# Optimization experiments

Measured on AMD Instinct MI355X. Metric: run time of the kernel, lower is better.

Reference implementation:

```python
import jax, jax.numpy as jnp
import numpy as np

N_NODES = 100000
N_EDGES = 1600000
NFEAT = 128
NHID = 64
DROPOUT = 0.5


def setup_inputs() -> dict:
    key = jax.random.key(0)
    k1, k2, k3, k4, k5, k6 = jax.random.split(key, 6)
    x = jax.random.normal(k1, (N_NODES, NFEAT), dtype=jnp.float32)
    edge_row = jax.random.randint(k2, (N_EDGES,), 0, N_NODES, dtype=jnp.int32)
    edge_col = jax.random.randint(k3, (N_EDGES,), 0, N_NODES, dtype=jnp.int32)
    edge_val = jax.random.uniform(k4, (N_EDGES,), dtype=jnp.float32)
    # GraphConvolution params (uniform init as in Kipf's reference impl)
    stdv = 1.0 / np.sqrt(NHID)
    W = jax.random.uniform(k5, (NFEAT, NHID), minval=-stdv, maxval=stdv, dtype=jnp.float32)
    b = jax.random.uniform(k6, (NHID,), minval=-stdv, maxval=stdv, dtype=jnp.float32)
    return {"x": x, "edge_row": edge_row, "edge_col": edge_col,
            "edge_val": edge_val, "W": W, "b": b}


def reference(x, edge_row, edge_col, edge_val, W, b):
    # GraphConvolution: support = x @ W ; out = spmm(adj, support) + b
    support = x @ W                                   # [N, nhid]
    msgs = edge_val[:, None] * support[edge_col]       # gather: [E, nhid]
    agg = jax.ops.segment_sum(msgs, edge_row, num_segments=N_NODES)  # scatter-add
    h = jax.nn.relu(agg + b)
    # F.dropout(p=0.5, training=True): inverted dropout with fixed mask
    keep = 1.0 - DROPOUT
    mask = jax.random.bernoulli(jax.random.key(42), keep, h.shape)
    return jnp.where(mask, h / keep, 0.0)
```

## Files before the change

kernel.cpp:

```cpp
#include <hip/hip_runtime.h>

#define N_NODES 100000
#define N_EDGES 1600000
#define NFEAT 128
#define NHID 64

#define BBITS 8
#define NBUCK 391
#define BATCH 4096
#define NBATCH ((N_EDGES + BATCH - 1) / BATCH)
#define NREP 4
#define RSTRIDE 1536
#define HCAP 2560
#define CMASK 0x1FFFF

typedef __attribute__((ext_vector_type(8))) short short8;
typedef __attribute__((ext_vector_type(4))) float f32x4;

__device__ __forceinline__ unsigned short f2bf(float f) {
  unsigned u = __float_as_uint(f);
  u += 0x7fffu + ((u >> 16) & 1u);
  return (unsigned short)(u >> 16);
}

__global__ __launch_bounds__(256) void gcn_wt(const float* __restrict__ W,
                                              unsigned short* __restrict__ wt,
                                              int* __restrict__ cursor) {
  const int i = blockIdx.x * 256 + threadIdx.x;
  const int n = i >> 7;
  const int k = i & 127;
  wt[i] = f2bf(W[k * NHID + n]);
  if (blockIdx.x == 0)
    for (int b = threadIdx.x; b < NBUCK * NREP; b += 256)
      cursor[b * 16] = 0;
}

__global__ __launch_bounds__(256) void gcn_gemm(const float* __restrict__ x,
                                                const unsigned short* __restrict__ wt,
                                                unsigned short* __restrict__ support_h) {
  __shared__ float ldsx[64 * NFEAT];
  const int t = threadIdx.x;
  const int node0 = blockIdx.x * 64;
  const float4* __restrict__ gx = (const float4*)(x + (size_t)node0 * NFEAT);
  float4* lx4 = (float4*)ldsx;
  const int limit4 = (N_NODES - node0) * (NFEAT / 4);
#pragma unroll
  for (int i = 0; i < 8; ++i) {
    const int idx = i * 256 + t;
    if (idx < limit4) lx4[idx] = gx[idx];
  }
  __syncthreads();
  const int wv = t >> 6;
  const int lane = t & 63;
  const int quad = lane >> 4;
  const int nl = lane & 15;
  const int mrow = wv * 16 + nl;
  f32x4 acc[4];
#pragma unroll
  for (int nt = 0; nt < 4; ++nt)
#pragma unroll
    for (int r = 0; r < 4; ++r) acc[nt][r] = 0.f;
#pragma unroll
  for (int kc = 0; kc < 4; ++kc) {
    const float* ap = &ldsx[mrow * NFEAT + kc * 32 + quad * 8];
    const float4 a0 = *(const float4*)ap;
    const float4 a1 = *(const float4*)(ap + 4);
    union { short8 v; unsigned short s[8]; } au;
    au.s[0] = f2bf(a0.x); au.s[1] = f2bf(a0.y);
    au.s[2] = f2bf(a0.z); au.s[3] = f2bf(a0.w);
    au.s[4] = f2bf(a1.x); au.s[5] = f2bf(a1.y);
    au.s[6] = f2bf(a1.z); au.s[7] = f2bf(a1.w);
#pragma unroll
    for (int nt = 0; nt < 4; ++nt) {
      const short8 bf = *(const short8*)(wt + (size_t)(nt * 16 + nl) * NFEAT +
                                         kc * 32 + quad * 8);
      acc[nt] = __builtin_amdgcn_mfma_f32_16x16x32_bf16(au.v, bf, acc[nt], 0, 0, 0);
    }
  }
#pragma unroll
  for (int nt = 0; nt < 4; ++nt)
#pragma unroll
    for (int r = 0; r < 4; ++r) {
      const int node = node0 + wv * 16 + quad * 4 + r;
      if (node < N_NODES)
        support_h[(size_t)node * NHID + nt * 16 + nl] = f2bf(acc[nt][r]);
    }
}

__global__ __launch_bounds__(512) void gcn_bin(const int* __restrict__ erow,
                                               const int* __restrict__ ecol,
                                               const float* __restrict__ eval_,
                                               int* __restrict__ cursor,
                                               int2* __restrict__ eg) {
  __shared__ int h[NBUCK];
  __shared__ int ofs[NBUCK];
  __shared__ int wsum[8];
  __shared__ int spx[BATCH];
  __shared__ int sv[BATCH];
  __shared__ short sb[BATCH];
  const int t = threadIdx.x;
  const int rep = blockIdx.x & (NREP - 1);
  if (t < NBUCK) h[t] = 0;
  __syncthreads();
  const int base = blockIdx.x * BATCH;
  const int n = min(BATCH, N_EDGES - base);
  int mypx[8], myv[8], myrank[8], myb[8];
#pragma unroll
  for (int u = 0; u < 8; ++u) {
    const int j = t + u * 512;
    if (j < n) {
      const int r = erow[base + j];
      mypx[u] = ((r & 255) << 17) | ecol[base + j];
      myv[u] = __float_as_int(eval_[base + j]);
      myb[u] = r >> BBITS;
      myrank[u] = atomicAdd(&h[myb[u]], 1);
    }
  }
  __syncthreads();
  const int hv = (t < NBUCK) ? h[t] : 0;
  const int lane = t & 63;
  int v = hv;
#pragma unroll
  for (int off = 1; off < 64; off <<= 1) {
    const int u = __shfl_up(v, off);
    if (lane >= off) v += u;
  }
  if (lane == 63) wsum[t >> 6] = v;
  __syncthreads();
  int wbase = 0;
  const int mywv = t >> 6;
  for (int w = 0; w < mywv; ++w) wbase += wsum[w];
  const int my_ofs = wbase + v - hv;
  if (t < NBUCK) {
    ofs[t] = my_ofs;
    const int c = hv;
    if (c > 0) {
      const int old = atomicAdd(&cursor[(t * NREP + rep) * 16], c);
      h[t] = (t * NREP + rep) * RSTRIDE + old - my_ofs;
    }
  }
  __syncthreads();
#pragma unroll
  for (int u = 0; u < 8; ++u) {
    const int j = t + u * 512;
    if (j < n) {
      const int pos = ofs[myb[u]] + myrank[u];
      spx[pos] = mypx[u];
      sv[pos] = myv[u];
      sb[pos] = (short)myb[u];
    }
  }
  __syncthreads();
  for (int j = t; j < n; j += 512) {
    const int d = h[sb[j]] + j;
    eg[d] = make_int2(spx[j], sv[j]);
  }
}

__device__ __forceinline__ unsigned rotl32(unsigned v, int r) {
  return (v << r) | (v >> (32 - r));
}

__device__ __forceinline__ unsigned threefry_draw(unsigned i) {
  const unsigned ks0 = 0u;
  const unsigned ks1 = 42u;
  const unsigned ks2 = 0x1BD11BDAu ^ 42u;
  unsigned x0 = 0u + ks0;
  unsigned x1 = i + ks1;
#define TF_ROUND(r) { x0 += x1; x1 = rotl32(x1, (r)); x1 ^= x0; }
  TF_ROUND(13) TF_ROUND(15) TF_ROUND(26) TF_ROUND(6)
  x0 += ks1; x1 += ks2 + 1u;
  TF_ROUND(17) TF_ROUND(29) TF_ROUND(16) TF_ROUND(24)
  x0 += ks2; x1 += ks0 + 2u;
  TF_ROUND(13) TF_ROUND(15) TF_ROUND(26) TF_ROUND(6)
  x0 += ks0; x1 += ks1 + 3u;
  TF_ROUND(17) TF_ROUND(29) TF_ROUND(16) TF_ROUND(24)
  x0 += ks1; x1 += ks2 + 4u;
  TF_ROUND(13) TF_ROUND(15) TF_ROUND(26) TF_ROUND(6)
  x0 += ks2; x1 += ks0 + 5u;
#undef TF_ROUND
  return x0 ^ x1;
}

__global__ __launch_bounds__(512) void gcn_rowagg(const int* __restrict__ cursor,
                                                  const int2* __restrict__ eg,
                                                  const unsigned short* __restrict__ support_h,
                                                  const float* __restrict__ b,
                                                  float* __restrict__ out) {
  __shared__ int2 srec[HCAP];
  __shared__ int cnt[128];
  __shared__ int rstart[128];
  const int t = threadIdx.x;
  const int k = blockIdx.x >> 1;
  const int half = blockIdx.x & 1;
  if (t < 128) cnt[t] = 0;
  __syncthreads();
  int px[12], pv[12], rk[12];
  int idx = 0;
#pragma unroll
  for (int rep = 0; rep < NREP; ++rep) {
    const int span = k * NREP + rep;
    const int n = cursor[span * 16];
    const int sbase = span * RSTRIDE;
#pragma unroll
    for (int u = 0; u < 3; ++u, ++idx) {
      const int j = t + u * 512;
      const bool ok = j < n;
      int2 p = make_int2(0, 0);
      if (ok) p = eg[sbase + j];
      px[idx] = p.x;
      pv[idx] = p.y;
      const int r = ((unsigned)p.x) >> 17;
      rk[idx] = (ok && ((r >> 7) == half)) ? atomicAdd(&cnt[r & 127], 1) : -1;
    }
  }
  __syncthreads();
  if (t < 64) {
    const int a0 = cnt[t];
    const int a1 = cnt[64 + t];
    int s0 = a0;
#pragma unroll
    for (int off = 1; off < 64; off <<= 1) {
      const int u = __shfl_up(s0, off);
      if (t >= off) s0 += u;
    }
    const int tot0 = __shfl(s0, 63);
    int s1 = a1;
#pragma unroll
    for (int off = 1; off < 64; off <<= 1) {
      const int u = __shfl_up(s1, off);
      if (t >= off) s1 += u;
    }
    rstart[t] = s0 - a0;
    rstart[64 + t] = tot0 + s1 - a1;
  }
  __syncthreads();
#pragma unroll
  for (int u = 0; u < 12; ++u) {
    if (rk[u] >= 0) {
      const int r = (((unsigned)px[u]) >> 17) & 127;
      srec[rstart[r] + rk[u]] = make_int2(px[u] & CMASK, pv[u]);
    }
  }
  __syncthreads();
  const int wv = t >> 6;
  const int lane = t & 63;
  const int grp = lane >> 3;
  const int sub = lane & 7;
  const int feat = (sub << 3) | grp;
  const float bias = b[feat];
  for (int rr = 0; rr < 16; ++rr) {
    const int r = wv * 16 + rr;
    const int node = (k << BBITS) + (half << 7) + r;
    if (node >= N_NODES) break;
    const int s = rstart[r];
    const int e = s + cnt[r];
    float acc[8];
#pragma unroll
    for (int j = 0; j < 8; ++j) acc[j] = 0.f;
    for (int i = s; i < e; i += 8) {
      const int ii = i + grp;
      int2 p = make_int2(0, 0);
      if (ii < e) p = srec[ii];
      const uint4 q = ((const uint4*)support_h)[(size_t)p.x * 8 + sub];
      const float v = __int_as_float(p.y);
      acc[0] = __builtin_fmaf(v, __uint_as_float(q.x << 16), acc[0]);
      acc[1] = __builtin_fmaf(v, __uint_as_float(q.x & 0xffff0000u), acc[1]);
      acc[2] = __builtin_fmaf(v, __uint_as_float(q.y << 16), acc[2]);
      acc[3] = __builtin_fmaf(v, __uint_as_float(q.y & 0xffff0000u), acc[3]);
      acc[4] = __builtin_fmaf(v, __uint_as_float(q.z << 16), acc[4]);
      acc[5] = __builtin_fmaf(v, __uint_as_float(q.z & 0xffff0000u), acc[5]);
      acc[6] = __builtin_fmaf(v, __uint_as_float(q.w << 16), acc[6]);
      acc[7] = __builtin_fmaf(v, __uint_as_float(q.w & 0xffff0000u), acc[7]);
    }
    const int g0 = grp & 1, g1 = (grp >> 1) & 1, g2 = grp >> 2;
    float v4[4];
#pragma unroll
    for (int i = 0; i < 4; ++i) {
      const float keep = g0 ? acc[2 * i + 1] : acc[2 * i];
      const float give = g0 ? acc[2 * i] : acc[2 * i + 1];
      v4[i] = keep + __shfl_xor(give, 8);
    }
    float v2[2];
#pragma unroll
    for (int i = 0; i < 2; ++i) {
      const float keep = g1 ? v4[2 * i + 1] : v4[2 * i];
      const float give = g1 ? v4[2 * i] : v4[2 * i + 1];
      v2[i] = keep + __shfl_xor(give, 16);
    }
    const float keep = g2 ? v2[1] : v2[0];
    const float give = g2 ? v2[0] : v2[1];
    const float aval = keep + __shfl_xor(give, 32);
    const float h = fmaxf(aval + bias, 0.f);
    const unsigned idxg = (unsigned)node * 64u + (unsigned)feat;
    const bool keepm = (threefry_draw(idxg) >> 31) == 0u;
    out[idxg] = keepm ? h * 2.0f : 0.0f;
  }
}

extern "C" void kernel_launch(void* const* d_in, const int* in_sizes, int n_in,
                              void* d_out, int out_size, void* d_ws, size_t ws_size,
                              hipStream_t stream) {
  const float* x     = (const float*)d_in[0];
  const int*   erow  = (const int*)d_in[1];
  const int*   ecol  = (const int*)d_in[2];
  const float* eval_ = (const float*)d_in[3];
  const float* W     = (const float*)d_in[4];
  const float* b     = (const float*)d_in[5];
  float* out = (float*)d_out;

  char* ws = (char*)d_ws;
  unsigned short* support_h = (unsigned short*)(ws);
  unsigned short* wt        = (unsigned short*)(ws + 12800000);
  int*  cursor  = (int*)(ws + 12816384);
  int2* eg      = (int2*)(ws + 12916480);

  hipLaunchKernelGGL(gcn_wt, dim3(32), dim3(256), 0, stream, W, wt, cursor);
  hipLaunchKernelGGL(gcn_gemm, dim3((N_NODES + 63) / 64), dim3(256), 0, stream,
                     x, wt, support_h);
  hipLaunchKernelGGL(gcn_bin, dim3(NBATCH), dim3(512), 0, stream,
                     erow, ecol, eval_, cursor, eg);
  hipLaunchKernelGGL(gcn_rowagg, dim3(2 * NBUCK), dim3(512), 0, stream,
                     cursor, eg, support_h, b, out);
}
```

Measured before the change: 194.0 us.

## Fuse GEMM, binning and row aggregation into one cooperative persistent kernel

Replaces the four separate launches with one persistent cooperative kernel. Its first phase interleaves the GEMM tiles (now 128 nodes, with W transposed to bf16 in LDS per tile) and the edge-binning batches, then a grid-wide sync precedes the row aggregation phase. The cursor reset moves to a memset. The aim is to cut launch gaps and tail effects and to let the GEMM overlap the binning. In exchange, every GEMM tile redoes the W conversion, the grid is capped by occupancy, and the grid sync plus cooperative launch add their own overhead.

```diff
diff --git a/kernel.cpp b/kernel.cpp
--- a/kernel.cpp
+++ b/kernel.cpp
@@ -1,4 +1,7 @@
 #include <hip/hip_runtime.h>
+#include <hip/hip_cooperative_groups.h>
+
+namespace cg = cooperative_groups;
 
 #define N_NODES 100000
 #define N_EDGES 1600000
@@ -8,11 +11,14 @@
 #define BBITS 8
 #define NBUCK 391
 #define BATCH 4096
-#define NBATCH ((N_EDGES + BATCH - 1) / BATCH)
+#define NBATCH 391
+#define NTILE 782
 #define NREP 4
 #define RSTRIDE 1536
 #define HCAP 2560
 #define CMASK 0x1FFFF
+#define XPITCH 136
+#define SH_BYTES 52224
 
 typedef __attribute__((ext_vector_type(8))) short short8;
 typedef __attribute__((ext_vector_type(4))) float f32x4;
@@ -21,140 +27,6 @@
   unsigned u = __float_as_uint(f);
   u += 0x7fffu + ((u >> 16) & 1u);
   return (unsigned short)(u >> 16);
-}
-
-__global__ __launch_bounds__(256) void gcn_wt(const float* __restrict__ W,
-                                              unsigned short* __restrict__ wt,
-                                              int* __restrict__ cursor) {
-  const int i = blockIdx.x * 256 + threadIdx.x;
-  const int n = i >> 7;
-  const int k = i & 127;
-  wt[i] = f2bf(W[k * NHID + n]);
-  if (blockIdx.x == 0)
-    for (int b = threadIdx.x; b < NBUCK * NREP; b += 256)
-      cursor[b * 16] = 0;
-}
-
-__global__ __launch_bounds__(256) void gcn_gemm(const float* __restrict__ x,
-                                                const unsigned short* __restrict__ wt,
-                                                unsigned short* __restrict__ support_h) {
-  __shared__ float ldsx[64 * NFEAT];
-  const int t = threadIdx.x;
-  const int node0 = blockIdx.x * 64;
-  const float4* __restrict__ gx = (const float4*)(x + (size_t)node0 * NFEAT);
-  float4* lx4 = (float4*)ldsx;
-  const int limit4 = (N_NODES - node0) * (NFEAT / 4);
-#pragma unroll
-  for (int i = 0; i < 8; ++i) {
-    const int idx = i * 256 + t;
-    if (idx < limit4) lx4[idx] = gx[idx];
-  }
-  __syncthreads();
-  const int wv = t >> 6;
-  const int lane = t & 63;
-  const int quad = lane >> 4;
-  const int nl = lane & 15;
-  const int mrow = wv * 16 + nl;
-  f32x4 acc[4];
-#pragma unroll
-  for (int nt = 0; nt < 4; ++nt)
-#pragma unroll
-    for (int r = 0; r < 4; ++r) acc[nt][r] = 0.f;
-#pragma unroll
-  for (int kc = 0; kc < 4; ++kc) {
-    const float* ap = &ldsx[mrow * NFEAT + kc * 32 + quad * 8];
-    const float4 a0 = *(const float4*)ap;
-    const float4 a1 = *(const float4*)(ap + 4);
-    union { short8 v; unsigned short s[8]; } au;
-    au.s[0] = f2bf(a0.x); au.s[1] = f2bf(a0.y);
-    au.s[2] = f2bf(a0.z); au.s[3] = f2bf(a0.w);
-    au.s[4] = f2bf(a1.x); au.s[5] = f2bf(a1.y);
-    au.s[6] = f2bf(a1.z); au.s[7] = f2bf(a1.w);
-#pragma unroll
-    for (int nt = 0; nt < 4; ++nt) {
-      const short8 bf = *(const short8*)(wt + (size_t)(nt * 16 + nl) * NFEAT +
-                                         kc * 32 + quad * 8);
-      acc[nt] = __builtin_amdgcn_mfma_f32_16x16x32_bf16(au.v, bf, acc[nt], 0, 0, 0);
-    }
-  }
-#pragma unroll
-  for (int nt = 0; nt < 4; ++nt)
-#pragma unroll
-    for (int r = 0; r < 4; ++r) {
-      const int node = node0 + wv * 16 + quad * 4 + r;
-      if (node < N_NODES)
-        support_h[(size_t)node * NHID + nt * 16 + nl] = f2bf(acc[nt][r]);
-    }
-}
-
-__global__ __launch_bounds__(512) void gcn_bin(const int* __restrict__ erow,
-                                               const int* __restrict__ ecol,
-                                               const float* __restrict__ eval_,
-                                               int* __restrict__ cursor,
-                                               int2* __restrict__ eg) {
-  __shared__ int h[NBUCK];
-  __shared__ int ofs[NBUCK];
-  __shared__ int wsum[8];
-  __shared__ int spx[BATCH];
-  __shared__ int sv[BATCH];
-  __shared__ short sb[BATCH];
-  const int t = threadIdx.x;
-  const int rep = blockIdx.x & (NREP - 1);
-  if (t < NBUCK) h[t] = 0;
-  __syncthreads();
-  const int base = blockIdx.x * BATCH;
-  const int n = min(BATCH, N_EDGES - base);
-  int mypx[8], myv[8], myrank[8], myb[8];
-#pragma unroll
-  for (int u = 0; u < 8; ++u) {
-    const int j = t + u * 512;
-    if (j < n) {
-      const int r = erow[base + j];
-      mypx[u] = ((r & 255) << 17) | ecol[base + j];
-      myv[u] = __float_as_int(eval_[base + j]);
-      myb[u] = r >> BBITS;
-      myrank[u] = atomicAdd(&h[myb[u]], 1);
-    }
-  }
-  __syncthreads();
-  const int hv = (t < NBUCK) ? h[t] : 0;
-  const int lane = t & 63;
-  int v = hv;
-#pragma unroll
-  for (int off = 1; off < 64; off <<= 1) {
-    const int u = __shfl_up(v, off);
-    if (lane >= off) v += u;
-  }
-  if (lane == 63) wsum[t >> 6] = v;
-  __syncthreads();
-  int wbase = 0;
-  const int mywv = t >> 6;
-  for (int w = 0; w < mywv; ++w) wbase += wsum[w];
-  const int my_ofs = wbase + v - hv;
-  if (t < NBUCK) {
-    ofs[t] = my_ofs;
-    const int c = hv;
-    if (c > 0) {
-      const int old = atomicAdd(&cursor[(t * NREP + rep) * 16], c);
-      h[t] = (t * NREP + rep) * RSTRIDE + old - my_ofs;
-    }
-  }
-  __syncthreads();
-#pragma unroll
-  for (int u = 0; u < 8; ++u) {
-    const int j = t + u * 512;
-    if (j < n) {
-      const int pos = ofs[myb[u]] + myrank[u];
-      spx[pos] = mypx[u];
-      sv[pos] = myv[u];
-      sb[pos] = (short)myb[u];
-    }
-  }
-  __syncthreads();
-  for (int j = t; j < n; j += 512) {
-    const int d = h[sb[j]] + j;
-    eg[d] = make_int2(spx[j], sv[j]);
-  }
 }
 
 __device__ __forceinline__ unsigned rotl32(unsigned v, int r) {
@@ -182,119 +54,247 @@
   return x0 ^ x1;
 }
 
-__global__ __launch_bounds__(512) void gcn_rowagg(const int* __restrict__ cursor,
-                                                  const int2* __restrict__ eg,
-                                                  const unsigned short* __restrict__ support_h,
-                                                  const float* __restrict__ b,
-                                                  float* __restrict__ out) {
-  __shared__ int2 srec[HCAP];
-  __shared__ int cnt[128];
-  __shared__ int rstart[128];
+__global__ void __launch_bounds__(512, 6) gcn_mega(
+    const float* __restrict__ x, const int* __restrict__ erow,
+    const int* __restrict__ ecol, const float* __restrict__ eval_,
+    const float* __restrict__ W, const float* __restrict__ bias_g,
+    float* __restrict__ out, unsigned short* __restrict__ support_h,
+    int* __restrict__ cursor, int2* __restrict__ eg) {
+  __shared__ __align__(16) char shraw[SH_BYTES];
   const int t = threadIdx.x;
-  const int k = blockIdx.x >> 1;
-  const int half = blockIdx.x & 1;
-  if (t < 128) cnt[t] = 0;
-  __syncthreads();
-  int px[12], pv[12], rk[12];
-  int idx = 0;
-#pragma unroll
-  for (int rep = 0; rep < NREP; ++rep) {
-    const int span = k * NREP + rep;
-    const int n = cursor[span * 16];
-    const int sbase = span * RSTRIDE;
-#pragma unroll
-    for (int u = 0; u < 3; ++u, ++idx) {
-      const int j = t + u * 512;
-      const bool ok = j < n;
-      int2 p = make_int2(0, 0);
-      if (ok) p = eg[sbase + j];
-      px[idx] = p.x;
-      pv[idx] = p.y;
-      const int r = ((unsigned)p.x) >> 17;
-      rk[idx] = (ok && ((r >> 7) == half)) ? atomicAdd(&cnt[r & 127], 1) : -1;
-    }
+  cg::grid_group grid = cg::this_grid();
+
+  for (int u = blockIdx.x; u < NTILE + NBATCH; u += gridDim.x) {
+    __syncthreads();
+    if (u < NTILE) {
+      unsigned short* xbf = (unsigned short*)shraw;
+      unsigned short* wtb = (unsigned short*)(shraw + 34816);
+      const int node0 = u * 128;
+      for (int i = t; i < NHID * NFEAT; i += 512) {
+        const int k = i >> 6;
+        const int n = i & 63;
+        wtb[n * XPITCH + k] = f2bf(W[i]);
+      }
+      const int limf4 = min(128, N_NODES - node0) * 32;
+      const float4* gx = (const float4*)(x + (size_t)node0 * NFEAT);
+      for (int i = t; i < 128 * 32; i += 512) {
+        if (i < limf4) {
+          const float4 v = gx[i];
+          ushort4 o;
+          o.x = f2bf(v.x); o.y = f2bf(v.y); o.z = f2bf(v.z); o.w = f2bf(v.w);
+          *(ushort4*)(xbf + (i >> 5) * XPITCH + (i & 31) * 4) = o;
+        }
+      }
+      __syncthreads();
+      const int wv = t >> 6;
+      const int lane = t & 63;
+      const int quad = lane >> 4;
+      const int nl = lane & 15;
+      const int mrow = wv * 16 + nl;
+      f32x4 acc[4];
+#pragma unroll
+      for (int nt = 0; nt < 4; ++nt)
+#pragma unroll
+        for (int r = 0; r < 4; ++r) acc[nt][r] = 0.f;
+#pragma unroll
+      for (int kc = 0; kc < 4; ++kc) {
+        const short8 a = *(const short8*)(xbf + mrow * XPITCH + kc * 32 + quad * 8);
+#pragma unroll
+        for (int nt = 0; nt < 4; ++nt) {
+          const short8 bf = *(const short8*)(wtb + (nt * 16 + nl) * XPITCH +
+                                             kc * 32 + quad * 8);
+          acc[nt] = __builtin_amdgcn_mfma_f32_16x16x32_bf16(a, bf, acc[nt], 0, 0, 0);
+        }
+      }
+#pragma unroll
+      for (int nt = 0; nt < 4; ++nt)
+#pragma unroll
+        for (int r = 0; r < 4; ++r) {
+          const int node = node0 + wv * 16 + quad * 4 + r;
+          if (node < N_NODES)
+            support_h[(size_t)node * NHID + nt * 16 + nl] = f2bf(acc[nt][r]);
+        }
+    } else {
+      int* h    = (int*)shraw;
+      int* ofs  = (int*)(shraw + 1568);
+      int* wsum = (int*)(shraw + 3136);
+      int* spx  = (int*)(shraw + 3168);
+      int* sv   = (int*)(shraw + 19552);
+      short* sb = (short*)(shraw + 35936);
+      const int bidx = u - NTILE;
+      const int rep = bidx & (NREP - 1);
+      if (t < NBUCK) h[t] = 0;
+      __syncthreads();
+      const int base = bidx * BATCH;
+      const int n = min(BATCH, N_EDGES - base);
+      int mypx[8], myv[8], myrank[8], myb[8];
+#pragma unroll
+      for (int v = 0; v < 8; ++v) {
+        const int j = t + v * 512;
+        if (j < n) {
+          const int r = erow[base + j];
+          mypx[v] = ((r & 255) << 17) | ecol[base + j];
+          myv[v] = __float_as_int(eval_[base + j]);
+          myb[v] = r >> BBITS;
+          myrank[v] = atomicAdd(&h[myb[v]], 1);
+        }
+      }
+      __syncthreads();
+      const int hv = (t < NBUCK) ? h[t] : 0;
+      const int lane = t & 63;
+      int v = hv;
+#pragma unroll
+      for (int off = 1; off < 64; off <<= 1) {
+        const int uu = __shfl_up(v, off);
+        if (lane >= off) v += uu;
+      }
+      if (lane == 63) wsum[t >> 6] = v;
+      __syncthreads();
+      int wbase = 0;
+      const int mywv = t >> 6;
+      for (int w = 0; w < mywv; ++w) wbase += wsum[w];
+      const int my_ofs = wbase + v - hv;
+      if (t < NBUCK) {
+        ofs[t] = my_ofs;
+        const int c = hv;
+        if (c > 0) {
+          const int old = atomicAdd(&cursor[(t * NREP + rep) * 16], c);
+          h[t] = (t * NREP + rep) * RSTRIDE + old - my_ofs;
+        }
+      }
+      __syncthreads();
+#pragma unroll
+      for (int vv = 0; vv < 8; ++vv) {
+        const int j = t + vv * 512;
+        if (j < n) {
+          const int pos = ofs[myb[vv]] + myrank[vv];
+          spx[pos] = mypx[vv];
+          sv[pos] = myv[vv];
+          sb[pos] = (short)myb[vv];
+        }
+      }
+      __syncthreads();
+      for (int j = t; j < n; j += 512) {
+        const int d = h[sb[j]] + j;
+        eg[d] = make_int2(spx[j], sv[j]);
+      }
+    }
+    __syncthreads();
   }
-  __syncthreads();
-  if (t < 64) {
-    const int a0 = cnt[t];
-    const int a1 = cnt[64 + t];
-    int s0 = a0;
-#pragma unroll
-    for (int off = 1; off < 64; off <<= 1) {
-      const int u = __shfl_up(s0, off);
-      if (t >= off) s0 += u;
-    }
-    const int tot0 = __shfl(s0, 63);
-    int s1 = a1;
-#pragma unroll
-    for (int off = 1; off < 64; off <<= 1) {
-      const int u = __shfl_up(s1, off);
-      if (t >= off) s1 += u;
-    }
-    rstart[t] = s0 - a0;
-    rstart[64 + t] = tot0 + s1 - a1;
-  }
-  __syncthreads();
-#pragma unroll
-  for (int u = 0; u < 12; ++u) {
-    if (rk[u] >= 0) {
-      const int r = (((unsigned)px[u]) >> 17) & 127;
-      srec[rstart[r] + rk[u]] = make_int2(px[u] & CMASK, pv[u]);
-    }
-  }
-  __syncthreads();
-  const int wv = t >> 6;
-  const int lane = t & 63;
-  const int grp = lane >> 3;
-  const int sub = lane & 7;
-  const int feat = (sub << 3) | grp;
-  const float bias = b[feat];
-  for (int rr = 0; rr < 16; ++rr) {
-    const int r = wv * 16 + rr;
-    const int node = (k << BBITS) + (half << 7) + r;
-    if (node >= N_NODES) break;
-    const int s = rstart[r];
-    const int e = s + cnt[r];
-    float acc[8];
-#pragma unroll
-    for (int j = 0; j < 8; ++j) acc[j] = 0.f;
-    for (int i = s; i < e; i += 8) {
-      const int ii = i + grp;
-      int2 p = make_int2(0, 0);
-      if (ii < e) p = srec[ii];
-      const uint4 q = ((const uint4*)support_h)[(size_t)p.x * 8 + sub];
-      const float v = __int_as_float(p.y);
-      acc[0] = __builtin_fmaf(v, __uint_as_float(q.x << 16), acc[0]);
-      acc[1] = __builtin_fmaf(v, __uint_as_float(q.x & 0xffff0000u), acc[1]);
-      acc[2] = __builtin_fmaf(v, __uint_as_float(q.y << 16), acc[2]);
-      acc[3] = __builtin_fmaf(v, __uint_as_float(q.y & 0xffff0000u), acc[3]);
-      acc[4] = __builtin_fmaf(v, __uint_as_float(q.z << 16), acc[4]);
-      acc[5] = __builtin_fmaf(v, __uint_as_float(q.z & 0xffff0000u), acc[5]);
-      acc[6] = __builtin_fmaf(v, __uint_as_float(q.w << 16), acc[6]);
-      acc[7] = __builtin_fmaf(v, __uint_as_float(q.w & 0xffff0000u), acc[7]);
-    }
-    const int g0 = grp & 1, g1 = (grp >> 1) & 1, g2 = grp >> 2;
-    float v4[4];
-#pragma unroll
-    for (int i = 0; i < 4; ++i) {
-      const float keep = g0 ? acc[2 * i + 1] : acc[2 * i];
-      const float give = g0 ? acc[2 * i] : acc[2 * i + 1];
-      v4[i] = keep + __shfl_xor(give, 8);
-    }
-    float v2[2];
-#pragma unroll
-    for (int i = 0; i < 2; ++i) {
-      const float keep = g1 ? v4[2 * i + 1] : v4[2 * i];
-      const float give = g1 ? v4[2 * i] : v4[2 * i + 1];
-      v2[i] = keep + __shfl_xor(give, 16);
-    }
-    const float keep = g2 ? v2[1] : v2[0];
-    const float give = g2 ? v2[0] : v2[1];
-    const float aval = keep + __shfl_xor(give, 32);
-    const float h = fmaxf(aval + bias, 0.f);
-    const unsigned idxg = (unsigned)node * 64u + (unsigned)feat;
-    const bool keepm = (threefry_draw(idxg) >> 31) == 0u;
-    out[idxg] = keepm ? h * 2.0f : 0.0f;
+
+  grid.sync();
+
+  for (int u = blockIdx.x; u < 2 * NBUCK; u += gridDim.x) {
+    __syncthreads();
+    int2* srec  = (int2*)shraw;
+    int* cnt    = (int*)(shraw + 20480);
+    int* rstart = (int*)(shraw + 20992);
+    const int k = u >> 1;
+    const int half = u & 1;
+    if (t < 128) cnt[t] = 0;
+    __syncthreads();
+    int px[12], pv[12], rk[12];
+    int idx = 0;
+#pragma unroll
+    for (int rep = 0; rep < NREP; ++rep) {
+      const int span = k * NREP + rep;
+      const int n = cursor[span * 16];
+      const int sbase = span * RSTRIDE;
+#pragma unroll
+      for (int uu = 0; uu < 3; ++uu, ++idx) {
+        const int j = t + uu * 512;
+        const bool ok = j < n;
+        int2 p = make_int2(0, 0);
+        if (ok) p = eg[sbase + j];
+        px[idx] = p.x;
+        pv[idx] = p.y;
+        const int r = ((unsigned)p.x) >> 17;
+        rk[idx] = (ok && ((r >> 7) == half)) ? atomicAdd(&cnt[r & 127], 1) : -1;
+      }
+    }
+    __syncthreads();
+    if (t < 64) {
+      const int a0 = cnt[t];
+      const int a1 = cnt[64 + t];
+      int s0 = a0;
+#pragma unroll
+      for (int off = 1; off < 64; off <<= 1) {
+        const int uu = __shfl_up(s0, off);
+        if (t >= off) s0 += uu;
+      }
+      const int tot0 = __shfl(s0, 63);
+      int s1 = a1;
+#pragma unroll
+      for (int off = 1; off < 64; off <<= 1) {
+        const int uu = __shfl_up(s1, off);
+        if (t >= off) s1 += uu;
+      }
+      rstart[t] = s0 - a0;
+      rstart[64 + t] = tot0 + s1 - a1;
+    }
+    __syncthreads();
+#pragma unroll
+    for (int uu = 0; uu < 12; ++uu) {
+      if (rk[uu] >= 0) {
+        const int r = (((unsigned)px[uu]) >> 17) & 127;
+        srec[rstart[r] + rk[uu]] = make_int2(px[uu] & CMASK, pv[uu]);
+      }
+    }
+    __syncthreads();
+    const int wv = t >> 6;
+    const int lane = t & 63;
+    const int grp = lane >> 3;
+    const int sub = lane & 7;
+    const int feat = (sub << 3) | grp;
+    const float bias = bias_g[feat];
+    for (int rr = 0; rr < 16; ++rr) {
+      const int r = wv * 16 + rr;
+      const int node = (k << BBITS) + (half << 7) + r;
+      if (node >= N_NODES) break;
+      const int s = rstart[r];
+      const int e = s + cnt[r];
+      float acc[8];
+#pragma unroll
+      for (int j = 0; j < 8; ++j) acc[j] = 0.f;
+      for (int i = s; i < e; i += 8) {
+        const int ii = i + grp;
+        int2 p = make_int2(0, 0);
+        if (ii < e) p = srec[ii];
+        const uint4 q = ((const uint4*)support_h)[(size_t)p.x * 8 + sub];
+        const float v = __int_as_float(p.y);
+        acc[0] = __builtin_fmaf(v, __uint_as_float(q.x << 16), acc[0]);
+        acc[1] = __builtin_fmaf(v, __uint_as_float(q.x & 0xffff0000u), acc[1]);
+        acc[2] = __builtin_fmaf(v, __uint_as_float(q.y << 16), acc[2]);
+        acc[3] = __builtin_fmaf(v, __uint_as_float(q.y & 0xffff0000u), acc[3]);
+        acc[4] = __builtin_fmaf(v, __uint_as_float(q.z << 16), acc[4]);
+        acc[5] = __builtin_fmaf(v, __uint_as_float(q.z & 0xffff0000u), acc[5]);
+        acc[6] = __builtin_fmaf(v, __uint_as_float(q.w << 16), acc[6]);
+        acc[7] = __builtin_fmaf(v, __uint_as_float(q.w & 0xffff0000u), acc[7]);
+      }
+      const int g0 = grp & 1, g1 = (grp >> 1) & 1, g2 = grp >> 2;
+      float v4[4];
+#pragma unroll
+      for (int i = 0; i < 4; ++i) {
+        const float keep = g0 ? acc[2 * i + 1] : acc[2 * i];
+        const float give = g0 ? acc[2 * i] : acc[2 * i + 1];
+        v4[i] = keep + __shfl_xor(give, 8);
+      }
+      float v2[2];
+#pragma unroll
+      for (int i = 0; i < 2; ++i) {
+        const float keep = g1 ? v4[2 * i + 1] : v4[2 * i];
+        const float give = g1 ? v4[2 * i] : v4[2 * i + 1];
+        v2[i] = keep + __shfl_xor(give, 16);
+      }
+      const float keep = g2 ? v2[1] : v2[0];
+      const float give = g2 ? v2[0] : v2[1];
+      const float aval = keep + __shfl_xor(give, 32);
+      const float h = fmaxf(aval + bias, 0.f);
+      const unsigned idxg = (unsigned)node * 64u + (unsigned)feat;
+      const bool keepm = (threefry_draw(idxg) >> 31) == 0u;
+      out[idxg] = keepm ? h * 2.0f : 0.0f;
+    }
+    __syncthreads();
   }
 }
 
@@ -311,15 +311,20 @@
 
   char* ws = (char*)d_ws;
   unsigned short* support_h = (unsigned short*)(ws);
-  unsigned short* wt        = (unsigned short*)(ws + 12800000);
-  int*  cursor  = (int*)(ws + 12816384);
-  int2* eg      = (int2*)(ws + 12916480);
-
-  hipLaunchKernelGGL(gcn_wt, dim3(32), dim3(256), 0, stream, W, wt, cursor);
-  hipLaunchKernelGGL(gcn_gemm, dim3((N_NODES + 63) / 64), dim3(256), 0, stream,
-                     x, wt, support_h);
-  hipLaunchKernelGGL(gcn_bin, dim3(NBATCH), dim3(512), 0, stream,
-                     erow, ecol, eval_, cursor, eg);
-  hipLaunchKernelGGL(gcn_rowagg, dim3(2 * NBUCK), dim3(512), 0, stream,
-                     cursor, eg, support_h, b, out);
-}
+  int*  cursor = (int*)(ws + 12800000);
+  int2* eg     = (int2*)(ws + 12900096);
+
+  hipMemsetAsync(cursor, 0, NBUCK * NREP * 16 * sizeof(int), stream);
+
+  int maxb = 0;
+  hipOccupancyMaxActiveBlocksPerMultiprocessor(&maxb, (const void*)gcn_mega, 512, 0);
+  if (maxb < 1) maxb = 1;
+  if (maxb > 3) maxb = 3;
+  const int grid = maxb * 256;
+
+  void* args[] = {(void*)&x, (void*)&erow, (void*)&ecol, (void*)&eval_,
+                  (void*)&W, (void*)&b, (void*)&out, (void*)&support_h,
+                  (void*)&cursor, (void*)&eg};
+  hipLaunchCooperativeKernel((const void*)gcn_mega, dim3(grid), dim3(512),
+                             args, 0, stream);
+}
```

Measured after the change: 321.7 us. 1.66x slower.

## Fuse weight transpose into GEMM, store bf16 x in LDS, split rowagg into quarters

Applied to the files above, without the earlier changes.

Removes the separate weight-transpose kernel: each GEMM block now converts W to bf16 and transposes it into padded LDS itself, and it also zeroes the cursors. The x tile is converted to bf16 once during staging, which shrinks LDS use and drops the per-MFMA conversion. The row-aggregation kernel is split into four blocks per bucket instead of two, with smaller LDS record buffers, to raise parallelism. The cost is redundant W conversion in every GEMM block, and more rowagg blocks that each re-read the bucket's edge records. NBATCH is hardcoded to 391, the same value as before.

```diff
diff --git a/kernel.cpp b/kernel.cpp
--- a/kernel.cpp
+++ b/kernel.cpp
@@ -8,11 +8,12 @@
 #define BBITS 8
 #define NBUCK 391
 #define BATCH 4096
-#define NBATCH ((N_EDGES + BATCH - 1) / BATCH)
+#define NBATCH 391
 #define NREP 4
 #define RSTRIDE 1536
-#define HCAP 2560
+#define QCAP 1408
 #define CMASK 0x1FFFF
+#define XP 132
 
 typedef __attribute__((ext_vector_type(8))) short short8;
 typedef __attribute__((ext_vector_type(4))) float f32x4;
@@ -23,31 +24,30 @@
   return (unsigned short)(u >> 16);
 }
 
-__global__ __launch_bounds__(256) void gcn_wt(const float* __restrict__ W,
-                                              unsigned short* __restrict__ wt,
-                                              int* __restrict__ cursor) {
-  const int i = blockIdx.x * 256 + threadIdx.x;
-  const int n = i >> 7;
-  const int k = i & 127;
-  wt[i] = f2bf(W[k * NHID + n]);
+__global__ __launch_bounds__(256) void gcn_gemm(const float* __restrict__ x,
+                                                const float* __restrict__ W,
+                                                unsigned short* __restrict__ support_h,
+                                                int* __restrict__ cursor) {
+  __shared__ unsigned short xbf[64 * XP];
+  __shared__ unsigned short wtb[64 * XP];
+  const int t = threadIdx.x;
   if (blockIdx.x == 0)
-    for (int b = threadIdx.x; b < NBUCK * NREP; b += 256)
-      cursor[b * 16] = 0;
-}
-
-__global__ __launch_bounds__(256) void gcn_gemm(const float* __restrict__ x,
-                                                const unsigned short* __restrict__ wt,
-                                                unsigned short* __restrict__ support_h) {
-  __shared__ float ldsx[64 * NFEAT];
-  const int t = threadIdx.x;
+    for (int i = t; i < NBUCK * NREP; i += 256) cursor[i * 16] = 0;
+  for (int i = t; i < NHID * NFEAT; i += 256) {
+    const int k = i >> 6;
+    const int n = i & 63;
+    wtb[n * XP + k] = f2bf(W[i]);
+  }
   const int node0 = blockIdx.x * 64;
   const float4* __restrict__ gx = (const float4*)(x + (size_t)node0 * NFEAT);
-  float4* lx4 = (float4*)ldsx;
-  const int limit4 = (N_NODES - node0) * (NFEAT / 4);
-#pragma unroll
-  for (int i = 0; i < 8; ++i) {
-    const int idx = i * 256 + t;
-    if (idx < limit4) lx4[idx] = gx[idx];
+  const int limf4 = min(64, N_NODES - node0) * 32;
+  for (int i = t; i < 64 * 32; i += 256) {
+    if (i < limf4) {
+      const float4 v = gx[i];
+      ushort4 o;
+      o.x = f2bf(v.x); o.y = f2bf(v.y); o.z = f2bf(v.z); o.w = f2bf(v.w);
+      *(ushort4*)(xbf + (i >> 5) * XP + (i & 31) * 4) = o;
+    }
   }
   __syncthreads();
   const int wv = t >> 6;
@@ -62,19 +62,11 @@
     for (int r = 0; r < 4; ++r) acc[nt][r] = 0.f;
 #pragma unroll
   for (int kc = 0; kc < 4; ++kc) {
-    const float* ap = &ldsx[mrow * NFEAT + kc * 32 + quad * 8];
-    const float4 a0 = *(const float4*)ap;
-    const float4 a1 = *(const float4*)(ap + 4);
-    union { short8 v; unsigned short s[8]; } au;
-    au.s[0] = f2bf(a0.x); au.s[1] = f2bf(a0.y);
-    au.s[2] = f2bf(a0.z); au.s[3] = f2bf(a0.w);
-    au.s[4] = f2bf(a1.x); au.s[5] = f2bf(a1.y);
-    au.s[6] = f2bf(a1.z); au.s[7] = f2bf(a1.w);
+    const short8 a = *(const short8*)(xbf + mrow * XP + kc * 32 + quad * 8);
 #pragma unroll
     for (int nt = 0; nt < 4; ++nt) {
-      const short8 bf = *(const short8*)(wt + (size_t)(nt * 16 + nl) * NFEAT +
-                                         kc * 32 + quad * 8);
-      acc[nt] = __builtin_amdgcn_mfma_f32_16x16x32_bf16(au.v, bf, acc[nt], 0, 0, 0);
+      const short8 bf = *(const short8*)(wtb + (nt * 16 + nl) * XP + kc * 32 + quad * 8);
+      acc[nt] = __builtin_amdgcn_mfma_f32_16x16x32_bf16(a, bf, acc[nt], 0, 0, 0);
     }
   }
 #pragma unroll
@@ -187,13 +179,13 @@
                                                   const unsigned short* __restrict__ support_h,
                                                   const float* __restrict__ b,
                                                   float* __restrict__ out) {
-  __shared__ int2 srec[HCAP];
-  __shared__ int cnt[128];
-  __shared__ int rstart[128];
+  __shared__ int2 srec[QCAP];
+  __shared__ int cnt[64];
+  __shared__ int rstart[64];
   const int t = threadIdx.x;
-  const int k = blockIdx.x >> 1;
-  const int half = blockIdx.x & 1;
-  if (t < 128) cnt[t] = 0;
+  const int k = blockIdx.x >> 2;
+  const int qtr = blockIdx.x & 3;
+  if (t < 64) cnt[t] = 0;
   __syncthreads();
   int px[12], pv[12], rk[12];
   int idx = 0;
@@ -211,34 +203,25 @@
       px[idx] = p.x;
       pv[idx] = p.y;
       const int r = ((unsigned)p.x) >> 17;
-      rk[idx] = (ok && ((r >> 7) == half)) ? atomicAdd(&cnt[r & 127], 1) : -1;
+      rk[idx] = (ok && ((r >> 6) == qtr)) ? atomicAdd(&cnt[r & 63], 1) : -1;
     }
   }
   __syncthreads();
   if (t < 64) {
-    const int a0 = cnt[t];
-    const int a1 = cnt[64 + t];
-    int s0 = a0;
+    const int a = cnt[t];
+    int s = a;
 #pragma unroll
     for (int off = 1; off < 64; off <<= 1) {
-      const int u = __shfl_up(s0, off);
-      if (t >= off) s0 += u;
-    }
-    const int tot0 = __shfl(s0, 63);
-    int s1 = a1;
-#pragma unroll
-    for (int off = 1; off < 64; off <<= 1) {
-      const int u = __shfl_up(s1, off);
-      if (t >= off) s1 += u;
-    }
-    rstart[t] = s0 - a0;
-    rstart[64 + t] = tot0 + s1 - a1;
+      const int u = __shfl_up(s, off);
+      if (t >= off) s += u;
+    }
+    rstart[t] = s - a;
   }
   __syncthreads();
 #pragma unroll
   for (int u = 0; u < 12; ++u) {
     if (rk[u] >= 0) {
-      const int r = (((unsigned)px[u]) >> 17) & 127;
+      const int r = (((unsigned)px[u]) >> 17) & 63;
       srec[rstart[r] + rk[u]] = make_int2(px[u] & CMASK, pv[u]);
     }
   }
@@ -249,9 +232,9 @@
   const int sub = lane & 7;
   const int feat = (sub << 3) | grp;
   const float bias = b[feat];
-  for (int rr = 0; rr < 16; ++rr) {
-    const int r = wv * 16 + rr;
-    const int node = (k << BBITS) + (half << 7) + r;
+  for (int rr = 0; rr < 8; ++rr) {
+    const int r = wv * 8 + rr;
+    const int node = (k << BBITS) + (qtr << 6) + r;
     if (node >= N_NODES) break;
     const int s = rstart[r];
     const int e = s + cnt[r];
@@ -311,15 +294,13 @@
 
   char* ws = (char*)d_ws;
   unsigned short* support_h = (unsigned short*)(ws);
-  unsigned short* wt        = (unsigned short*)(ws + 12800000);
-  int*  cursor  = (int*)(ws + 12816384);
-  int2* eg      = (int2*)(ws + 12916480);
-
-  hipLaunchKernelGGL(gcn_wt, dim3(32), dim3(256), 0, stream, W, wt, cursor);
+  int*  cursor = (int*)(ws + 12800000);
+  int2* eg     = (int2*)(ws + 12900096);
+
   hipLaunchKernelGGL(gcn_gemm, dim3((N_NODES + 63) / 64), dim3(256), 0, stream,
-                     x, wt, support_h);
+                     x, W, support_h, cursor);
   hipLaunchKernelGGL(gcn_bin, dim3(NBATCH), dim3(512), 0, stream,
                      erow, ecol, eval_, cursor, eg);
-  hipLaunchKernelGGL(gcn_rowagg, dim3(2 * NBUCK), dim3(512), 0, stream,
+  hipLaunchKernelGGL(gcn_rowagg, dim3(4 * NBUCK), dim3(512), 0, stream,
                      cursor, eg, support_h, b, out);
 }
```

After: 179.4 us. 1.08x faster.
